# Kernel optimization log

Hardware: AMD Instinct MI355X
Metric: run time of the kernel (lower is better)

The kernel has to match this reference:

```python
import jax, jax.numpy as jnp
import numpy as np

T = 512          # tokens
H = 2048         # hidden_size
E = 256          # n_routed_experts (8 groups x 32)
G = 8            # tucker groups
EPG = 32         # experts per group
K = 6            # top_k
I = 1408         # moe_intermediate_size
R1 = 128         # tucker input rank
R2 = 128         # tucker output rank


def setup_inputs() -> dict:
    key = jax.random.key(0)
    ks = jax.random.split(key, 12)
    s = 0.02
    return {
        "hidden_states": jax.random.normal(ks[0], (T, H), jnp.float32),
        "w_router": jax.random.normal(ks[1], (H, E), jnp.float32) * s,
        # gate_proj Tucker factors: H -> I
        "U_in_gate": jax.random.normal(ks[2], (G, H, R1), jnp.float32) * s,
        "core_gate": jax.random.normal(ks[3], (E, R1, R2), jnp.float32) * s,
        "U_out_gate": jax.random.normal(ks[4], (G, I, R2), jnp.float32) * s,
        # up_proj Tucker factors: H -> I
        "U_in_up": jax.random.normal(ks[5], (G, H, R1), jnp.float32) * s,
        "core_up": jax.random.normal(ks[6], (E, R1, R2), jnp.float32) * s,
        "U_out_up": jax.random.normal(ks[7], (G, I, R2), jnp.float32) * s,
        # down_proj Tucker factors: I -> H
        "U_in_down": jax.random.normal(ks[8], (G, I, R1), jnp.float32) * s,
        "core_down": jax.random.normal(ks[9], (E, R1, R2), jnp.float32) * s,
        "U_out_down": jax.random.normal(ks[10], (G, H, R2), jnp.float32) * s,
    }


def _tucker_apply(x, g, e, U_in, core, U_out):
    """Per-expert Tucker linear: y_t = ((x_t @ U_in[g_t]) @ core[e_t]) @ U_out[g_t].T
    x: [Td, din]; g: [Td] group ids; e: [Td] full expert ids.
    U_in: [G, din, r1]; core: [E, r1, r2]; U_out: [G, dout, r2]."""
    h1 = jnp.einsum('td,gdr->tgr', x, U_in)                       # [Td, G, r1]
    h1 = jnp.take_along_axis(h1, g[:, None, None], axis=1)[:, 0]  # [Td, r1]
    h2 = jnp.einsum('tr,trs->ts', h1, core[e])                    # [Td, r2]
    y = jnp.einsum('ts,gds->tgd', h2, U_out)                      # [Td, G, dout]
    return jnp.take_along_axis(y, g[:, None, None], axis=1)[:, 0]


def reference(hidden_states, w_router, U_in_gate, core_gate, U_out_gate,
              U_in_up, core_up, U_out_up, U_in_down, core_down, U_out_down):
    n_tok, hid = hidden_states.shape
    router_logits = hidden_states @ w_router                          # [T, E]
    probs = jax.nn.softmax(router_logits.astype(jnp.float32), axis=-1)
    routing_weights, selected = jax.lax.top_k(probs, K)               # [T, K]
    routing_weights = routing_weights / routing_weights.sum(-1, keepdims=True)
    routing_weights = routing_weights.astype(hidden_states.dtype)

    xd = jnp.repeat(hidden_states, K, axis=0)                         # [T*K, H]
    e = selected.reshape(-1)                                          # [T*K]
    g = e // EPG                                                      # group ids

    gate_out = _tucker_apply(xd, g, e, U_in_gate, core_gate, U_out_gate)
    up_out = _tucker_apply(xd, g, e, U_in_up, core_up, U_out_up)
    inter = jax.nn.silu(gate_out) * up_out                            # [T*K, I]
    down_out = _tucker_apply(inter, g, e, U_in_down, core_down, U_out_down)

    combined = (down_out.reshape(n_tok, K, hid) * routing_weights[..., None]).sum(axis=1)
    return combined
```

## Files before the change

### kernel.cpp

```cpp
#include <hip/hip_runtime.h>
#include <cmath>
#include <cstdint>

#define TNUM 512
#define HID 2048
#define NEXP 256
#define NGRP 8
#define KTOP 6
#define IDIM 1408
#define RNK 128
#define NPAIR (TNUM*KTOP)
#define NRCAP 3328
#define MAXTILES (NRCAP/32)

typedef _Float16 f16;
typedef f16  f16x8 __attribute__((ext_vector_type(8)));
typedef f16  f16x4 __attribute__((ext_vector_type(4)));
typedef float f32x4 __attribute__((ext_vector_type(4)));
#define MFMA16(a,b,c) __builtin_amdgcn_mfma_f32_16x16x32_f16((a),(b),(c),0,0,0)

static __device__ __forceinline__ float4 ld4(const float* p){ return *reinterpret_cast<const float4*>(p); }
static __device__ __forceinline__ void st4(float* p, float4 v){ *reinterpret_cast<float4*>(p) = v; }
static __device__ __forceinline__ f16x8 ldh8(const f16* p){ return *reinterpret_cast<const f16x8*>(p); }

constexpr size_t A256(size_t x){ return (x + 255) & ~(size_t)255; }
constexpr size_t OFF_SEL    = 0;
constexpr size_t OFF_WT     = A256(OFF_SEL    + (size_t)NPAIR*4);
constexpr size_t OFF_CNT    = A256(OFF_WT     + (size_t)NPAIR*4);
constexpr size_t OFF_ESTART = A256(OFF_CNT    + (size_t)NEXP*4);
constexpr size_t OFF_ECUR   = A256(OFF_ESTART + (size_t)NEXP*4);
constexpr size_t OFF_TG     = A256(OFF_ECUR   + (size_t)NEXP*4);
constexpr size_t OFF_HDR    = A256(OFF_TG     + (size_t)MAXTILES*4);
constexpr size_t OFF_ROWT   = A256(OFF_HDR    + 16);
constexpr size_t OFF_POS    = A256(OFF_ROWT   + (size_t)NRCAP*4);
constexpr size_t OFF_BIG    = A256(OFF_POS    + (size_t)NPAIR*4);

constexpr size_t SZ_XH    = (size_t)TNUM*HID*2;
constexpr size_t SZ_UTI   = (size_t)NGRP*RNK*HID*2;
constexpr size_t SZ_CT    = (size_t)NEXP*RNK*RNK*2;
constexpr size_t SZ_H1ALL = (size_t)2*TNUM*NGRP*RNK*2;
constexpr size_t SZ_UO    = (size_t)NGRP*IDIM*RNK*2;
constexpr size_t SZ_UOD   = (size_t)NGRP*HID*RNK*2;
constexpr size_t SZ_H2    = (size_t)NRCAP*RNK*2;
constexpr size_t SZ_INTER = (size_t)NRCAP*IDIM*2;
constexpr size_t SZ_DOWNO = (size_t)NRCAP*HID*4;

constexpr size_t OFF_XH    = OFF_BIG;
constexpr size_t OFF_UTIG  = OFF_XH   + SZ_XH;
constexpr size_t OFF_UTIU  = OFF_UTIG + SZ_UTI;
constexpr size_t OFF_CGT   = OFF_UTIU + SZ_UTI;
constexpr size_t OFF_CUT   = OFF_CGT  + SZ_CT;
constexpr size_t OFF_H1    = OFF_CUT  + SZ_CT;
constexpr size_t REG_END   = OFF_H1   + SZ_H1ALL;
constexpr size_t OFF_INTER = OFF_XH;
constexpr size_t OFF_DOWNO = OFF_XH;
constexpr size_t OFF_LPART = OFF_H1;
constexpr size_t OFF_UOG   = REG_END;
constexpr size_t OFF_UOU   = OFF_UOG  + SZ_UO;
constexpr size_t OFF_UTID  = OFF_UOU  + SZ_UO;
constexpr size_t OFF_UOD   = OFF_UTID + SZ_UO;
constexpr size_t OFF_CDT   = OFF_UOD  + SZ_UOD;
constexpr size_t OFF_H2G   = OFF_CDT  + SZ_CT;
constexpr size_t OFF_H2U   = OFF_H2G  + SZ_H2;
constexpr size_t OFF_D1    = OFF_H2U  + SZ_H2;
constexpr size_t OFF_D2    = OFF_D1   + SZ_H2;
constexpr size_t WS_NEED   = OFF_D2   + SZ_H2;
static_assert(OFF_DOWNO + SZ_DOWNO <= OFF_UOG, "downo overlay must end before persistent tail");
static_assert(OFF_INTER + SZ_INTER <= OFF_CGT, "inter overlay must end before cores");

__global__ __launch_bounds__(256) void k_cvt_all(
    const float* __restrict__ x,   const float* __restrict__ Uog,
    const float* __restrict__ Uou, const float* __restrict__ Uod,
    f16* __restrict__ xh, f16* __restrict__ uog, f16* __restrict__ uou, f16* __restrict__ uod){
  const int b = blockIdx.x, tid = threadIdx.x;
  const float* in; f16* hi; size_t i; float scale;
  if(b < 1024){        in = x;   hi = xh;  i = (size_t)b*256 + tid;        scale = 1.f; }
  else if(b < 2432){   in = Uog; hi = uog; i = (size_t)(b-1024)*256 + tid; scale = 16.f; }
  else if(b < 3840){   in = Uou; hi = uou; i = (size_t)(b-2432)*256 + tid; scale = 16.f; }
  else {               in = Uod; hi = uod; i = (size_t)(b-3840)*256 + tid; scale = 16.f; }
  float4 v = ld4(in + i*4);
  f16x4 H;
  H[0]=(f16)(v.x*scale); H[1]=(f16)(v.y*scale); H[2]=(f16)(v.z*scale); H[3]=(f16)(v.w*scale);
  *reinterpret_cast<f16x4*>(hi + i*4) = H;
}

__global__ __launch_bounds__(256) void k_cvt_t3(
    const float* __restrict__ Uig, const float* __restrict__ Uiu, const float* __restrict__ Uid,
    f16* __restrict__ ig, f16* __restrict__ iu, f16* __restrict__ idn){
  __shared__ float tile[32][33];
  const int z = blockIdx.z, tensor = z>>3, g = z&7;
  const float* in; f16* hi; int R;
  if(tensor == 0){ in = Uig; hi = ig; R = HID; }
  else if(tensor == 1){ in = Uiu; hi = iu; R = HID; }
  else { in = Uid; hi = idn; R = IDIM; }
  const int r0 = blockIdx.y*32, c0 = blockIdx.x*32;
  if(r0 >= R) return;
  const int tid = threadIdx.x;
  { const int r = tid>>3, c4 = (tid&7)*4;
    float4 v = ld4(in + ((size_t)g*R + r0 + r)*RNK + c0 + c4);
    tile[r][c4]=v.x; tile[r][c4+1]=v.y; tile[r][c4+2]=v.z; tile[r][c4+3]=v.w; }
  __syncthreads();
  { const int c = tid>>3, r4 = (tid&7)*4;
    f16x4 H;
    #pragma unroll
    for(int k = 0; k < 4; k++) H[k] = (f16)(tile[r4+k][c]*16.f);
    *reinterpret_cast<f16x4*>(hi + ((size_t)g*RNK + c0 + c)*R + r0 + r4) = H; }
}

__global__ __launch_bounds__(256) void k_cvt_core(
    const float* __restrict__ cg, const float* __restrict__ cu, const float* __restrict__ cd,
    f16* __restrict__ cgt, f16* __restrict__ cut, f16* __restrict__ cdt){
  __shared__ float tile[32][33];
  const int z = blockIdx.z, tensor = z>>8, e = z&255;
  const float* in; f16* o;
  if(tensor == 0){ in = cg; o = cgt; }
  else if(tensor == 1){ in = cu; o = cut; }
  else { in = cd; o = cdt; }
  in += (size_t)e*RNK*RNK; o += (size_t)e*RNK*RNK;
  const int r0 = blockIdx.y*32, c0 = blockIdx.x*32;
  const int tid = threadIdx.x;
  { const int r = tid>>3, c4 = (tid&7)*4;
    float4 v = ld4(in + (size_t)(r0+r)*RNK + c0 + c4);
    tile[r][c4]=v.x; tile[r][c4+1]=v.y; tile[r][c4+2]=v.z; tile[r][c4+3]=v.w; }
  __syncthreads();
  { const int c = tid>>3, r4 = (tid&7)*4;
    f16x4 H;
    #pragma unroll
    for(int k = 0; k < 4; k++) H[k] = (f16)(tile[r4+k][c]*16.f);
    *reinterpret_cast<f16x4*>(o + (size_t)(c0+c)*RNK + r0 + r4) = H; }
}

__global__ __launch_bounds__(256) void k_router4(const float* __restrict__ x,
                                                 const float* __restrict__ w,
                                                 float* __restrict__ lpart){
  __shared__ float As[32][68];
  __shared__ float Bs[64][64];
  const int tid = threadIdx.x;
  const int t0 = blockIdx.x*32, e0 = blockIdx.y*64, kz = blockIdx.z;
  const int kb = kz*512;
  const int tx = tid & 15, ty = tid >> 4;
  float acc[2][4] = {{0.f}};
  for(int kc = 0; kc < 512; kc += 64){
    { const int r = tid>>3, k4 = (tid&7)<<2;
      st4(&As[r][k4],      ld4(&x[(size_t)(t0+r)*HID + kb + kc + k4]));
      st4(&As[r][k4+32],   ld4(&x[(size_t)(t0+r)*HID + kb + kc + k4 + 32])); }
    #pragma unroll
    for(int i = 0; i < 4; i++){ int idx = tid + i*256; int kr = idx>>4, e4 = (idx&15)<<2;
      st4(&Bs[kr][e4], ld4(&w[(size_t)(kb+kc+kr)*NEXP + e0 + e4])); }
    __syncthreads();
    for(int kk = 0; kk < 64; kk++){
      float4 b = ld4(&Bs[kk][tx<<2]);
      float a0 = As[(ty<<1)][kk], a1 = As[(ty<<1)+1][kk];
      acc[0][0] += a0*b.x; acc[0][1] += a0*b.y; acc[0][2] += a0*b.z; acc[0][3] += a0*b.w;
      acc[1][0] += a1*b.x; acc[1][1] += a1*b.y; acc[1][2] += a1*b.z; acc[1][3] += a1*b.w;
    }
    __syncthreads();
  }
  #pragma unroll
  for(int r = 0; r < 2; r++)
    st4(&lpart[((size_t)kz*TNUM + t0 + (ty<<1) + r)*NEXP + e0 + (tx<<2)],
        make_float4(acc[r][0],acc[r][1],acc[r][2],acc[r][3]));
}

__global__ __launch_bounds__(256) void k_topk(const float* __restrict__ lpart,
                                              int* __restrict__ sel,
                                              float* __restrict__ wt,
                                              int* __restrict__ cnt){
  __shared__ float wv[4];
  __shared__ int   wi[4];
  __shared__ float swin[KTOP];
  __shared__ int   iwin[KTOP];
  const int t = blockIdx.x, tid = threadIdx.x;
  const int lane = tid & 63, wid = tid >> 6;
  const size_t base = (size_t)t*NEXP + tid;
  float v = lpart[base] + lpart[base + (size_t)TNUM*NEXP]
          + lpart[base + (size_t)2*TNUM*NEXP] + lpart[base + (size_t)3*TNUM*NEXP];
  for(int k = 0; k < KTOP; k++){
    float cv = v; int ci = tid;
    #pragma unroll
    for(int off = 1; off < 64; off <<= 1){
      float ov = __shfl_xor(cv, off);
      int   oi = __shfl_xor(ci, off);
      if(ov > cv || (ov == cv && oi < ci)){ cv = ov; ci = oi; }
    }
    if(lane == 0){ wv[wid] = cv; wi[wid] = ci; }
    __syncthreads();
    if(tid == 0){
      float bv = wv[0]; int bi = wi[0];
      #pragma unroll
      for(int w2 = 1; w2 < 4; w2++)
        if(wv[w2] > bv || (wv[w2] == bv && wi[w2] < bi)){ bv = wv[w2]; bi = wi[w2]; }
      swin[k] = bv; iwin[k] = bi;
    }
    __syncthreads();
    if(tid == iwin[k]) v = -INFINITY;
  }
  if(tid == 0){
    float mx = swin[0], s = 0.f, ww[KTOP];
    #pragma unroll
    for(int k = 0; k < KTOP; k++){ ww[k] = expf(swin[k]-mx); s += ww[k]; }
    float inv = 1.f/s;
    #pragma unroll
    for(int k = 0; k < KTOP; k++){
      sel[t*KTOP+k] = iwin[k];
      wt[t*KTOP+k]  = ww[k]*inv;
      atomicAdd(&cnt[iwin[k]], 1);
    }
  }
}

__global__ __launch_bounds__(256) void k_meta(const int* __restrict__ cnt,
                                              int* __restrict__ estart,
                                              int* __restrict__ ecursor,
                                              int* __restrict__ tile_group,
                                              int* __restrict__ hdr){
  __shared__ int scnt[256];
  __shared__ int gsum[8];
  __shared__ int g0[9];
  const int tid = threadIdx.x;
  scnt[tid] = cnt[tid];
  if(tid < 8) gsum[tid] = 0;
  __syncthreads();
  atomicAdd(&gsum[tid>>5], scnt[tid]);
  __syncthreads();
  if(tid == 0){
    int run = 0;
    for(int g = 0; g < 8; g++){ g0[g] = run; run += (gsum[g]+31) & ~31; }
    g0[8] = run; hdr[0] = run>>5; hdr[1] = run;
  }
  __syncthreads();
  int g = tid >> 5, s = g0[g];
  for(int i = (g<<5); i < tid; i++) s += scnt[i];
  estart[tid] = s; ecursor[tid] = s;
  const int nt = g0[8] >> 5;
  for(int t2 = tid; t2 < MAXTILES; t2 += 256){
    int gg = -1;
    if(t2 < nt){
      for(int g2 = 0; g2 < 8; g2++) if(t2*32 >= g0[g2] && t2*32 < g0[g2+1]) gg = g2;
    }
    tile_group[t2] = gg;
  }
}

__global__ __launch_bounds__(256) void k_scatter(const int* __restrict__ sel,
                                                 int* __restrict__ ecursor,
                                                 int* __restrict__ row_t,
                                                 int* __restrict__ pos_of_pair){
  const int p = blockIdx.x*256 + threadIdx.x;
  if(p >= NPAIR) return;
  const int e = sel[p];
  const int pos = atomicAdd(&ecursor[e], 1);
  row_t[pos] = p / KTOP;
  pos_of_pair[p] = pos;
}

__global__ __launch_bounds__(256) void k_mm_stage1(
    const f16* __restrict__ xh,
    const f16* __restrict__ Bg_, const f16* __restrict__ Bu_,
    f16* __restrict__ H1){
  __shared__ float red[4][32][64];
  const int m = blockIdx.x, nt = blockIdx.y;
  const int pu = nt>>4, g = (nt>>1)&7, ch = nt&1;
  const f16* B = (pu ? Bu_ : Bg_) + (size_t)g*RNK*HID + (size_t)ch*64*HID;
  const int tid = threadIdx.x;
  const int wid = tid>>6, lane = tid&63, q = lane>>4, id = lane&15;
  const int kb = wid*512;
  const int r0 = m*32;
  f32x4 acc[2][4];
  #pragma unroll
  for(int f = 0; f < 2; f++)
    #pragma unroll
    for(int c = 0; c < 4; c++) acc[f][c] = (f32x4){0.f,0.f,0.f,0.f};
  #pragma unroll 4
  for(int kk = 0; kk < 512; kk += 32){
    f16x8 a0 = ldh8(xh + (size_t)(r0+id)*HID    + kb + kk + q*8);
    f16x8 a1 = ldh8(xh + (size_t)(r0+16+id)*HID + kb + kk + q*8);
    #pragma unroll
    for(int c = 0; c < 4; c++){
      f16x8 b = ldh8(B + (size_t)(c*16+id)*HID + kb + kk + q*8);
      acc[0][c] = MFMA16(a0, b, acc[0][c]);
      acc[1][c] = MFMA16(a1, b, acc[1][c]);
    }
  }
  #pragma unroll
  for(int f = 0; f < 2; f++)
    #pragma unroll
    for(int c = 0; c < 4; c++)
      #pragma unroll
      for(int r = 0; r < 4; r++)
        red[wid][f*16 + q*4 + r][c*16 + id] = acc[f][c][r];
  __syncthreads();
  f16* out = H1 + (size_t)pu*TNUM*(NGRP*RNK);
  const int row = tid>>3, c8 = (tid&7)*8;
  f16x8 o8;
  #pragma unroll
  for(int j = 0; j < 8; j++)
    o8[j] = (f16)(red[0][row][c8+j] + red[1][row][c8+j] + red[2][row][c8+j] + red[3][row][c8+j]);
  *reinterpret_cast<f16x8*>(&out[(size_t)(r0+row)*(NGRP*RNK) + g*RNK + ch*64 + c8]) = o8;
}

__global__ __launch_bounds__(256) void k_core2(
    const f16* __restrict__ Cg, const f16* __restrict__ Cu,
    const f16* __restrict__ H1,
    const int* __restrict__ estart, const int* __restrict__ cnt,
    const int* __restrict__ row_t,
    f16* __restrict__ h2g, f16* __restrict__ h2u){
  const int e = blockIdx.x, up = blockIdx.y;
  const int n = cnt[e];
  if(n == 0) return;
  const int j0 = estart[e], g = e >> 5;
  const f16* C = (up ? Cu : Cg) + (size_t)e*RNK*RNK;
  const f16* A = H1 + (size_t)up*TNUM*(NGRP*RNK);
  f16* o = up ? h2u : h2g;
  const int tid = threadIdx.x;
  const int wid = tid>>6, lane = tid&63, q = lane>>4, id = lane&15;
  for(int rt = 0; rt*16 < n; rt++){
    const int jrow = j0 + rt*16 + id;
    const int jj = jrow < j0+n ? jrow : j0;
    const f16* arow = A + (size_t)row_t[jj]*(NGRP*RNK) + g*RNK;
    f32x4 acc0 = (f32x4){0.f,0.f,0.f,0.f};
    f32x4 acc1 = (f32x4){0.f,0.f,0.f,0.f};
    #pragma unroll
    for(int kk = 0; kk < RNK; kk += 32){
      f16x8 a = ldh8(arow + kk + q*8);
      f16x8 b0 = ldh8(C + (size_t)(wid*32 + id)*RNK      + kk + q*8);
      f16x8 b1 = ldh8(C + (size_t)(wid*32 + 16 + id)*RNK + kk + q*8);
      acc0 = MFMA16(a, b0, acc0);
      acc1 = MFMA16(a, b1, acc1);
    }
    #pragma unroll
    for(int r = 0; r < 4; r++){
      const int j = j0 + rt*16 + q*4 + r;
      if(j < j0+n){
        o[(size_t)j*RNK + wid*32 + id]      = (f16)acc0[r];
        o[(size_t)j*RNK + wid*32 + 16 + id] = (f16)acc1[r];
      }
    }
  }
}

__global__ __launch_bounds__(128) void k_mm_gateup(
    const f16* __restrict__ Ag, const f16* __restrict__ Au,
    const f16* __restrict__ Bg, const f16* __restrict__ Bu,
    const int* __restrict__ tg,
    f16* __restrict__ inter){
  const int g = tg[blockIdx.x];
  if(g < 0) return;
  const int j0 = blockIdx.x*32;
  const int tid = threadIdx.x;
  const int wid = tid>>6, lane = tid&63, q = lane>>4, id = lane&15;
  const int c0 = blockIdx.y*128 + wid*64;
  const size_t bbase = (size_t)g*IDIM*RNK;
  f32x4 accg[2][4], accu[2][4];
  #pragma unroll
  for(int f = 0; f < 2; f++)
    #pragma unroll
    for(int c = 0; c < 4; c++){ accg[f][c] = (f32x4){0.f,0.f,0.f,0.f}; accu[f][c] = (f32x4){0.f,0.f,0.f,0.f}; }
  #pragma unroll 2
  for(int kk = 0; kk < RNK; kk += 32){
    const size_t a0off = (size_t)(j0+id)*RNK    + kk + q*8;
    const size_t a1off = (size_t)(j0+16+id)*RNK + kk + q*8;
    f16x8 ag0 = ldh8(Ag + a0off), ag1 = ldh8(Ag + a1off);
    f16x8 au0 = ldh8(Au + a0off), au1 = ldh8(Au + a1off);
    #pragma unroll
    for(int c = 0; c < 4; c++){
      const size_t boff = bbase + (size_t)(c0 + c*16 + id)*RNK + kk + q*8;
      f16x8 bg = ldh8(Bg + boff);
      f16x8 bu = ldh8(Bu + boff);
      accg[0][c] = MFMA16(ag0, bg, accg[0][c]);
      accg[1][c] = MFMA16(ag1, bg, accg[1][c]);
      accu[0][c] = MFMA16(au0, bu, accu[0][c]);
      accu[1][c] = MFMA16(au1, bu, accu[1][c]);
    }
  }
  #pragma unroll
  for(int f = 0; f < 2; f++)
    #pragma unroll
    for(int c = 0; c < 4; c++)
      #pragma unroll
      for(int r = 0; r < 4; r++){
        float vg = accg[f][c][r] * (1.f/4096.f);
        float vu = accu[f][c][r] * (1.f/4096.f);
        float sv = vg/(1.f+expf(-vg))*vu*256.f;
        inter[(size_t)(j0 + f*16 + q*4 + r)*IDIM + c0 + c*16 + id] = (f16)sv;
      }
}

__global__ __launch_bounds__(256) void k_mm_down_in(
    const f16* __restrict__ A_, const f16* __restrict__ B_,
    const int* __restrict__ tg,
    f16* __restrict__ d1){
  __shared__ float red[4][32][64];
  const int g = tg[blockIdx.x];
  if(g < 0) return;
  const int j0 = blockIdx.x*32;
  const int ch = blockIdx.y;
  const f16* B = B_ + (size_t)g*RNK*IDIM + (size_t)ch*64*IDIM;
  const int tid = threadIdx.x;
  const int wid = tid>>6, lane = tid&63, q = lane>>4, id = lane&15;
  const int kb = wid*352;
  f32x4 acc[2][4];
  #pragma unroll
  for(int f = 0; f < 2; f++)
    #pragma unroll
    for(int c = 0; c < 4; c++) acc[f][c] = (f32x4){0.f,0.f,0.f,0.f};
  #pragma unroll 2
  for(int kk = 0; kk < 352; kk += 32){
    f16x8 a0 = ldh8(A_ + (size_t)(j0+id)*IDIM    + kb + kk + q*8);
    f16x8 a1 = ldh8(A_ + (size_t)(j0+16+id)*IDIM + kb + kk + q*8);
    #pragma unroll
    for(int c = 0; c < 4; c++){
      f16x8 b = ldh8(B + (size_t)(c*16+id)*IDIM + kb + kk + q*8);
      acc[0][c] = MFMA16(a0, b, acc[0][c]);
      acc[1][c] = MFMA16(a1, b, acc[1][c]);
    }
  }
  #pragma unroll
  for(int f = 0; f < 2; f++)
    #pragma unroll
    for(int c = 0; c < 4; c++)
      #pragma unroll
      for(int r = 0; r < 4; r++)
        red[wid][f*16 + q*4 + r][c*16 + id] = acc[f][c][r];
  __syncthreads();
  const int row = tid>>3, c8 = (tid&7)*8;
  f16x8 o8;
  #pragma unroll
  for(int j = 0; j < 8; j++)
    o8[j] = (f16)(red[0][row][c8+j] + red[1][row][c8+j] + red[2][row][c8+j] + red[3][row][c8+j]);
  *reinterpret_cast<f16x8*>(&d1[(size_t)(j0+row)*RNK + ch*64 + c8]) = o8;
}

__global__ __launch_bounds__(256) void k_core_down(
    const f16* __restrict__ Cd,
    const f16* __restrict__ d1,
    const int* __restrict__ estart, const int* __restrict__ cnt,
    f16* __restrict__ d2){
  const int e = blockIdx.x;
  const int n = cnt[e];
  if(n == 0) return;
  const int j0 = estart[e];
  const f16* C = Cd + (size_t)e*RNK*RNK;
  const int tid = threadIdx.x;
  const int wid = tid>>6, lane = tid&63, q = lane>>4, id = lane&15;
  for(int rt = 0; rt*16 < n; rt++){
    const int jrow = j0 + rt*16 + id;
    const int jj = jrow < j0+n ? jrow : j0;
    const f16* arow = d1 + (size_t)jj*RNK;
    f32x4 acc0 = (f32x4){0.f,0.f,0.f,0.f};
    f32x4 acc1 = (f32x4){0.f,0.f,0.f,0.f};
    #pragma unroll
    for(int kk = 0; kk < RNK; kk += 32){
      f16x8 a = ldh8(arow + kk + q*8);
      f16x8 b0 = ldh8(C + (size_t)(wid*32 + id)*RNK      + kk + q*8);
      f16x8 b1 = ldh8(C + (size_t)(wid*32 + 16 + id)*RNK + kk + q*8);
      acc0 = MFMA16(a, b0, acc0);
      acc1 = MFMA16(a, b1, acc1);
    }
    #pragma unroll
    for(int r = 0; r < 4; r++){
      const int j = j0 + rt*16 + q*4 + r;
      if(j < j0+n){
        d2[(size_t)j*RNK + wid*32 + id]      = (f16)acc0[r];
        d2[(size_t)j*RNK + wid*32 + 16 + id] = (f16)acc1[r];
      }
    }
  }
}

__global__ __launch_bounds__(128) void k_mm_down_out(
    const f16* __restrict__ A_, const f16* __restrict__ B_,
    const int* __restrict__ tg,
    float* __restrict__ downo){
  const int g = tg[blockIdx.x];
  if(g < 0) return;
  const int j0 = blockIdx.x*32;
  const f16* B = B_ + (size_t)g*HID*RNK;
  const int tid = threadIdx.x;
  const int wid = tid>>6, lane = tid&63, q = lane>>4, id = lane&15;
  const int c0 = blockIdx.y*128 + wid*64;
  f32x4 acc[2][4];
  #pragma unroll
  for(int f = 0; f < 2; f++)
    #pragma unroll
    for(int c = 0; c < 4; c++) acc[f][c] = (f32x4){0.f,0.f,0.f,0.f};
  #pragma unroll 2
  for(int kk = 0; kk < RNK; kk += 32){
    f16x8 a0 = ldh8(A_ + (size_t)(j0+id)*RNK    + kk + q*8);
    f16x8 a1 = ldh8(A_ + (size_t)(j0+16+id)*RNK + kk + q*8);
    #pragma unroll
    for(int c = 0; c < 4; c++){
      f16x8 b = ldh8(B + (size_t)(c0 + c*16 + id)*RNK + kk + q*8);
      acc[0][c] = MFMA16(a0, b, acc[0][c]);
      acc[1][c] = MFMA16(a1, b, acc[1][c]);
    }
  }
  #pragma unroll
  for(int f = 0; f < 2; f++)
    #pragma unroll
    for(int c = 0; c < 4; c++)
      #pragma unroll
      for(int r = 0; r < 4; r++)
        downo[(size_t)(j0 + f*16 + q*4 + r)*HID + c0 + c*16 + id] = acc[f][c][r]*(1.f/1048576.f);
}

__global__ __launch_bounds__(256) void k_combine(const float* __restrict__ downo,
                                                 const int* __restrict__ pos_of_pair,
                                                 const float* __restrict__ wt,
                                                 float* __restrict__ out){
  const int idx = blockIdx.x*256 + threadIdx.x;
  const int t  = idx >> 9;
  const int h4 = (idx & 511) << 2;
  float4 acc = make_float4(0.f,0.f,0.f,0.f);
  #pragma unroll
  for(int k = 0; k < KTOP; k++){
    const int p = t*KTOP + k;
    const float w = wt[p];
    const int pos = pos_of_pair[p];
    float4 v = ld4(&downo[(size_t)pos*HID + h4]);
    acc.x += w*v.x; acc.y += w*v.y; acc.z += w*v.z; acc.w += w*v.w;
  }
  st4(&out[(size_t)t*HID + h4], acc);
}

extern "C" void kernel_launch(void* const* d_in, const int* in_sizes, int n_in,
                              void* d_out, int out_size, void* d_ws, size_t ws_size,
                              hipStream_t stream){
  const float* x   = (const float*)d_in[0];
  const float* wr  = (const float*)d_in[1];
  const float* Uig = (const float*)d_in[2];
  const float* cg  = (const float*)d_in[3];
  const float* Uog = (const float*)d_in[4];
  const float* Uiu = (const float*)d_in[5];
  const float* cu  = (const float*)d_in[6];
  const float* Uou = (const float*)d_in[7];
  const float* Uid = (const float*)d_in[8];
  const float* cd  = (const float*)d_in[9];
  const float* Uod = (const float*)d_in[10];
  float* out = (float*)d_out;
  char* ws = (char*)d_ws;
  if(ws_size < WS_NEED) return;

  int*   sel    = (int*)  (ws + OFF_SEL);
  float* wt     = (float*)(ws + OFF_WT);
  int*   cnt    = (int*)  (ws + OFF_CNT);
  int*   estart = (int*)  (ws + OFF_ESTART);
  int*   ecur   = (int*)  (ws + OFF_ECUR);
  int*   tg     = (int*)  (ws + OFF_TG);
  int*   hdr    = (int*)  (ws + OFF_HDR);
  int*   row_t  = (int*)  (ws + OFF_ROWT);
  int*   pos    = (int*)  (ws + OFF_POS);
  float* lpart  = (float*)(ws + OFF_LPART);
  f16* xh    = (f16*)(ws + OFF_XH);
  f16* utig  = (f16*)(ws + OFF_UTIG);
  f16* utiu  = (f16*)(ws + OFF_UTIU);
  f16* cgt   = (f16*)(ws + OFF_CGT);
  f16* cut   = (f16*)(ws + OFF_CUT);
  f16* cdt   = (f16*)(ws + OFF_CDT);
  f16* H1    = (f16*)(ws + OFF_H1);
  f16* uog   = (f16*)(ws + OFF_UOG);
  f16* uou   = (f16*)(ws + OFF_UOU);
  f16* utid  = (f16*)(ws + OFF_UTID);
  f16* uod   = (f16*)(ws + OFF_UOD);
  f16* h2g   = (f16*)(ws + OFF_H2G);
  f16* h2u   = (f16*)(ws + OFF_H2U);
  f16* inter = (f16*)(ws + OFF_INTER);
  f16* d1    = (f16*)(ws + OFF_D1);
  f16* d2    = (f16*)(ws + OFF_D2);
  float* downo = (float*)(ws + OFF_DOWNO);

  hipMemsetAsync(cnt, 0, NEXP*sizeof(int), stream);

  k_router4  <<<dim3(16,4,4),      256, 0, stream>>>(x, wr, lpart);
  k_topk     <<<TNUM,              256, 0, stream>>>(lpart, sel, wt, cnt);
  k_meta     <<<1,                 256, 0, stream>>>(cnt, estart, ecur, tg, hdr);
  k_scatter  <<<12,                256, 0, stream>>>(sel, ecur, row_t, pos);

  k_cvt_all  <<<5888,              256, 0, stream>>>(x, Uog, Uou, Uod, xh, uog, uou, uod);
  k_cvt_t3   <<<dim3(4,64,24),     256, 0, stream>>>(Uig, Uiu, Uid, utig, utiu, utid);
  k_cvt_core <<<dim3(4,4,768),     256, 0, stream>>>(cg, cu, cd, cgt, cut, cdt);

  k_mm_stage1<<<dim3(16,32),       256, 0, stream>>>(xh, utig, utiu, H1);
  k_core2    <<<dim3(NEXP,2),      256, 0, stream>>>(cgt, cut, H1, estart, cnt, row_t, h2g, h2u);
  k_mm_gateup<<<dim3(MAXTILES,11), 128, 0, stream>>>(h2g, h2u, uog, uou, tg, inter);
  k_mm_down_in<<<dim3(MAXTILES,2), 256, 0, stream>>>(inter, utid, tg, d1);
  k_core_down<<<NEXP,              256, 0, stream>>>(cdt, d1, estart, cnt, d2);
  k_mm_down_out<<<dim3(MAXTILES,16),128,0, stream>>>(d2, uod, tg, downo);
  k_combine  <<<1024,              256, 0, stream>>>(downo, pos, wt, out);
}
```

Before: 155.7 us.

## Use split-fp16 MFMA router, fuse meta/scatter, fold combine into down_out atomics

Replaces the fp32 scalar router GEMM with an MFMA version that splits x and w_router into fp16 hi/lo pairs, using three products to keep near-fp32 accuracy for top-k selection. It adds a transposed hi/lo router weight conversion. It merges the meta and scatter kernels into one block that scatters row weights instead of pair positions. It removes the fp32 downo buffer and the combine kernel by having down_out atomically add weighted results into a zeroed output. This trades extra conversion work and atomic contention for less memory traffic and fewer launches, and makes the summation order nondeterministic.

```diff
diff --git a/kernel.cpp b/kernel.cpp
--- a/kernel.cpp
+++ b/kernel.cpp
@@ -28,12 +28,11 @@
 constexpr size_t OFF_WT     = A256(OFF_SEL    + (size_t)NPAIR*4);
 constexpr size_t OFF_CNT    = A256(OFF_WT     + (size_t)NPAIR*4);
 constexpr size_t OFF_ESTART = A256(OFF_CNT    + (size_t)NEXP*4);
-constexpr size_t OFF_ECUR   = A256(OFF_ESTART + (size_t)NEXP*4);
-constexpr size_t OFF_TG     = A256(OFF_ECUR   + (size_t)NEXP*4);
+constexpr size_t OFF_TG     = A256(OFF_ESTART + (size_t)NEXP*4);
 constexpr size_t OFF_HDR    = A256(OFF_TG     + (size_t)MAXTILES*4);
 constexpr size_t OFF_ROWT   = A256(OFF_HDR    + 16);
-constexpr size_t OFF_POS    = A256(OFF_ROWT   + (size_t)NRCAP*4);
-constexpr size_t OFF_BIG    = A256(OFF_POS    + (size_t)NPAIR*4);
+constexpr size_t OFF_ROWW   = A256(OFF_ROWT   + (size_t)NRCAP*4);
+constexpr size_t OFF_BIG    = A256(OFF_ROWW   + (size_t)NRCAP*4);
 
 constexpr size_t SZ_XH    = (size_t)TNUM*HID*2;
 constexpr size_t SZ_UTI   = (size_t)NGRP*RNK*HID*2;
@@ -41,47 +40,82 @@
 constexpr size_t SZ_H1ALL = (size_t)2*TNUM*NGRP*RNK*2;
 constexpr size_t SZ_UO    = (size_t)NGRP*IDIM*RNK*2;
 constexpr size_t SZ_UOD   = (size_t)NGRP*HID*RNK*2;
+constexpr size_t SZ_WR    = (size_t)NEXP*HID*2;
 constexpr size_t SZ_H2    = (size_t)NRCAP*RNK*2;
 constexpr size_t SZ_INTER = (size_t)NRCAP*IDIM*2;
-constexpr size_t SZ_DOWNO = (size_t)NRCAP*HID*4;
 
 constexpr size_t OFF_XH    = OFF_BIG;
-constexpr size_t OFF_UTIG  = OFF_XH   + SZ_XH;
+constexpr size_t OFF_XL    = OFF_XH   + SZ_XH;
+constexpr size_t OFF_UTIG  = OFF_XL   + SZ_XH;
 constexpr size_t OFF_UTIU  = OFF_UTIG + SZ_UTI;
 constexpr size_t OFF_CGT   = OFF_UTIU + SZ_UTI;
 constexpr size_t OFF_CUT   = OFF_CGT  + SZ_CT;
 constexpr size_t OFF_H1    = OFF_CUT  + SZ_CT;
 constexpr size_t REG_END   = OFF_H1   + SZ_H1ALL;
 constexpr size_t OFF_INTER = OFF_XH;
-constexpr size_t OFF_DOWNO = OFF_XH;
 constexpr size_t OFF_LPART = OFF_H1;
 constexpr size_t OFF_UOG   = REG_END;
 constexpr size_t OFF_UOU   = OFF_UOG  + SZ_UO;
 constexpr size_t OFF_UTID  = OFF_UOU  + SZ_UO;
 constexpr size_t OFF_UOD   = OFF_UTID + SZ_UO;
 constexpr size_t OFF_CDT   = OFF_UOD  + SZ_UOD;
-constexpr size_t OFF_H2G   = OFF_CDT  + SZ_CT;
+constexpr size_t OFF_WRH   = OFF_CDT  + SZ_CT;
+constexpr size_t OFF_WRL   = OFF_WRH  + SZ_WR;
+constexpr size_t OFF_H2G   = OFF_WRL  + SZ_WR;
 constexpr size_t OFF_H2U   = OFF_H2G  + SZ_H2;
 constexpr size_t OFF_D1    = OFF_H2U  + SZ_H2;
 constexpr size_t OFF_D2    = OFF_D1   + SZ_H2;
 constexpr size_t WS_NEED   = OFF_D2   + SZ_H2;
-static_assert(OFF_DOWNO + SZ_DOWNO <= OFF_UOG, "downo overlay must end before persistent tail");
 static_assert(OFF_INTER + SZ_INTER <= OFF_CGT, "inter overlay must end before cores");
+static_assert(SZ_H1ALL >= (size_t)4*TNUM*NEXP*4/2 || true, "");
 
 __global__ __launch_bounds__(256) void k_cvt_all(
     const float* __restrict__ x,   const float* __restrict__ Uog,
     const float* __restrict__ Uou, const float* __restrict__ Uod,
-    f16* __restrict__ xh, f16* __restrict__ uog, f16* __restrict__ uou, f16* __restrict__ uod){
+    f16* __restrict__ xh, f16* __restrict__ xl,
+    f16* __restrict__ uog, f16* __restrict__ uou, f16* __restrict__ uod){
   const int b = blockIdx.x, tid = threadIdx.x;
-  const float* in; f16* hi; size_t i; float scale;
-  if(b < 1024){        in = x;   hi = xh;  i = (size_t)b*256 + tid;        scale = 1.f; }
-  else if(b < 2432){   in = Uog; hi = uog; i = (size_t)(b-1024)*256 + tid; scale = 16.f; }
-  else if(b < 3840){   in = Uou; hi = uou; i = (size_t)(b-2432)*256 + tid; scale = 16.f; }
-  else {               in = Uod; hi = uod; i = (size_t)(b-3840)*256 + tid; scale = 16.f; }
+  if(b < 1024){
+    const size_t i = (size_t)b*256 + tid;
+    float4 v = ld4(x + i*4);
+    f16x4 H, L;
+    H[0]=(f16)v.x; L[0]=(f16)(v.x-(float)H[0]);
+    H[1]=(f16)v.y; L[1]=(f16)(v.y-(float)H[1]);
+    H[2]=(f16)v.z; L[2]=(f16)(v.z-(float)H[2]);
+    H[3]=(f16)v.w; L[3]=(f16)(v.w-(float)H[3]);
+    *reinterpret_cast<f16x4*>(xh + i*4) = H;
+    *reinterpret_cast<f16x4*>(xl + i*4) = L;
+    return;
+  }
+  const float* in; f16* hi; size_t i;
+  if(b < 2432){        in = Uog; hi = uog; i = (size_t)(b-1024)*256 + tid; }
+  else if(b < 3840){   in = Uou; hi = uou; i = (size_t)(b-2432)*256 + tid; }
+  else {               in = Uod; hi = uod; i = (size_t)(b-3840)*256 + tid; }
   float4 v = ld4(in + i*4);
   f16x4 H;
-  H[0]=(f16)(v.x*scale); H[1]=(f16)(v.y*scale); H[2]=(f16)(v.z*scale); H[3]=(f16)(v.w*scale);
+  H[0]=(f16)(v.x*16.f); H[1]=(f16)(v.y*16.f); H[2]=(f16)(v.z*16.f); H[3]=(f16)(v.w*16.f);
   *reinterpret_cast<f16x4*>(hi + i*4) = H;
+}
+
+__global__ __launch_bounds__(256) void k_cvt_wr(const float* __restrict__ w,
+                                                f16* __restrict__ wh, f16* __restrict__ wl){
+  __shared__ float tile[32][33];
+  const int r0 = blockIdx.y*32, c0 = blockIdx.x*32;
+  const int tid = threadIdx.x;
+  { const int r = tid>>3, c4 = (tid&7)*4;
+    float4 v = ld4(w + (size_t)(r0+r)*NEXP + c0 + c4);
+    tile[r][c4]=v.x; tile[r][c4+1]=v.y; tile[r][c4+2]=v.z; tile[r][c4+3]=v.w; }
+  __syncthreads();
+  { const int c = tid>>3, r4 = (tid&7)*4;
+    f16x4 H, L;
+    #pragma unroll
+    for(int k = 0; k < 4; k++){
+      float v = tile[r4+k][c]*16.f;
+      H[k] = (f16)v; L[k] = (f16)(v - (float)H[k]);
+    }
+    const size_t o = (size_t)(c0+c)*HID + r0 + r4;
+    *reinterpret_cast<f16x4*>(wh + o) = H;
+    *reinterpret_cast<f16x4*>(wl + o) = L; }
 }
 
 __global__ __launch_bounds__(256) void k_cvt_t3(
@@ -130,36 +164,56 @@
     *reinterpret_cast<f16x4*>(o + (size_t)(c0+c)*RNK + r0 + r4) = H; }
 }
 
-__global__ __launch_bounds__(256) void k_router4(const float* __restrict__ x,
-                                                 const float* __restrict__ w,
-                                                 float* __restrict__ lpart){
-  __shared__ float As[32][68];
-  __shared__ float Bs[64][64];
-  const int tid = threadIdx.x;
-  const int t0 = blockIdx.x*32, e0 = blockIdx.y*64, kz = blockIdx.z;
-  const int kb = kz*512;
-  const int tx = tid & 15, ty = tid >> 4;
-  float acc[2][4] = {{0.f}};
-  for(int kc = 0; kc < 512; kc += 64){
-    { const int r = tid>>3, k4 = (tid&7)<<2;
-      st4(&As[r][k4],      ld4(&x[(size_t)(t0+r)*HID + kb + kc + k4]));
-      st4(&As[r][k4+32],   ld4(&x[(size_t)(t0+r)*HID + kb + kc + k4 + 32])); }
-    #pragma unroll
-    for(int i = 0; i < 4; i++){ int idx = tid + i*256; int kr = idx>>4, e4 = (idx&15)<<2;
-      st4(&Bs[kr][e4], ld4(&w[(size_t)(kb+kc+kr)*NEXP + e0 + e4])); }
-    __syncthreads();
-    for(int kk = 0; kk < 64; kk++){
-      float4 b = ld4(&Bs[kk][tx<<2]);
-      float a0 = As[(ty<<1)][kk], a1 = As[(ty<<1)+1][kk];
-      acc[0][0] += a0*b.x; acc[0][1] += a0*b.y; acc[0][2] += a0*b.z; acc[0][3] += a0*b.w;
-      acc[1][0] += a1*b.x; acc[1][1] += a1*b.y; acc[1][2] += a1*b.z; acc[1][3] += a1*b.w;
-    }
-    __syncthreads();
-  }
-  #pragma unroll
-  for(int r = 0; r < 2; r++)
-    st4(&lpart[((size_t)kz*TNUM + t0 + (ty<<1) + r)*NEXP + e0 + (tx<<2)],
-        make_float4(acc[r][0],acc[r][1],acc[r][2],acc[r][3]));
+__global__ __launch_bounds__(256) void k_router_mfma(
+    const f16* __restrict__ xh, const f16* __restrict__ xl,
+    const f16* __restrict__ wh, const f16* __restrict__ wl,
+    float* __restrict__ lpart){
+  __shared__ float red[4][32][64];
+  const int m = blockIdx.x, ecol = blockIdx.y, kz = blockIdx.z;
+  const int tid = threadIdx.x;
+  const int wid = tid>>6, lane = tid&63, q = lane>>4, id = lane&15;
+  const int r0 = m*32, e0 = ecol*64;
+  const int kb = kz*512 + wid*128;
+  f32x4 acc[2][4];
+  #pragma unroll
+  for(int f = 0; f < 2; f++)
+    #pragma unroll
+    for(int c = 0; c < 4; c++) acc[f][c] = (f32x4){0.f,0.f,0.f,0.f};
+  #pragma unroll
+  for(int kk = 0; kk < 128; kk += 32){
+    const size_t a0 = (size_t)(r0+id)*HID    + kb + kk + q*8;
+    const size_t a1 = (size_t)(r0+16+id)*HID + kb + kk + q*8;
+    f16x8 ah0 = ldh8(xh + a0), al0 = ldh8(xl + a0);
+    f16x8 ah1 = ldh8(xh + a1), al1 = ldh8(xl + a1);
+    #pragma unroll
+    for(int c = 0; c < 4; c++){
+      const size_t bo = (size_t)(e0 + c*16 + id)*HID + kb + kk + q*8;
+      f16x8 bh = ldh8(wh + bo);
+      f16x8 bl = ldh8(wl + bo);
+      acc[0][c] = MFMA16(ah0, bh, acc[0][c]);
+      acc[0][c] = MFMA16(ah0, bl, acc[0][c]);
+      acc[0][c] = MFMA16(al0, bh, acc[0][c]);
+      acc[1][c] = MFMA16(ah1, bh, acc[1][c]);
+      acc[1][c] = MFMA16(ah1, bl, acc[1][c]);
+      acc[1][c] = MFMA16(al1, bh, acc[1][c]);
+    }
+  }
+  #pragma unroll
+  for(int f = 0; f < 2; f++)
+    #pragma unroll
+    for(int c = 0; c < 4; c++)
+      #pragma unroll
+      for(int r = 0; r < 4; r++)
+        red[wid][f*16 + q*4 + r][c*16 + id] = acc[f][c][r];
+  __syncthreads();
+  const int row = tid>>3, c8 = (tid&7)*8;
+  float o[8];
+  #pragma unroll
+  for(int j = 0; j < 8; j++)
+    o[j] = (red[0][row][c8+j] + red[1][row][c8+j] + red[2][row][c8+j] + red[3][row][c8+j])*0.0625f;
+  float* dst = &lpart[((size_t)kz*TNUM + r0 + row)*NEXP + e0 + c8];
+  st4(dst,     make_float4(o[0],o[1],o[2],o[3]));
+  st4(dst + 4, make_float4(o[4],o[5],o[6],o[7]));
 }
 
 __global__ __launch_bounds__(256) void k_topk(const float* __restrict__ lpart,
@@ -209,14 +263,14 @@
   }
 }
 
-__global__ __launch_bounds__(256) void k_meta(const int* __restrict__ cnt,
-                                              int* __restrict__ estart,
-                                              int* __restrict__ ecursor,
-                                              int* __restrict__ tile_group,
-                                              int* __restrict__ hdr){
+__global__ __launch_bounds__(256) void k_meta_scatter(
+    const int* __restrict__ cnt, const int* __restrict__ sel, const float* __restrict__ wt,
+    int* __restrict__ estart, int* __restrict__ tile_group, int* __restrict__ hdr,
+    int* __restrict__ row_t, float* __restrict__ row_w){
   __shared__ int scnt[256];
   __shared__ int gsum[8];
   __shared__ int g0[9];
+  __shared__ int curs[256];
   const int tid = threadIdx.x;
   scnt[tid] = cnt[tid];
   if(tid < 8) gsum[tid] = 0;
@@ -231,7 +285,7 @@
   __syncthreads();
   int g = tid >> 5, s = g0[g];
   for(int i = (g<<5); i < tid; i++) s += scnt[i];
-  estart[tid] = s; ecursor[tid] = s;
+  estart[tid] = s; curs[tid] = s;
   const int nt = g0[8] >> 5;
   for(int t2 = tid; t2 < MAXTILES; t2 += 256){
     int gg = -1;
@@ -240,18 +294,14 @@
     }
     tile_group[t2] = gg;
   }
-}
-
-__global__ __launch_bounds__(256) void k_scatter(const int* __restrict__ sel,
-                                                 int* __restrict__ ecursor,
-                                                 int* __restrict__ row_t,
-                                                 int* __restrict__ pos_of_pair){
-  const int p = blockIdx.x*256 + threadIdx.x;
-  if(p >= NPAIR) return;
-  const int e = sel[p];
-  const int pos = atomicAdd(&ecursor[e], 1);
-  row_t[pos] = p / KTOP;
-  pos_of_pair[p] = pos;
+  for(int i = tid; i < NRCAP; i += 256) row_w[i] = 0.f;
+  __syncthreads();
+  for(int p = tid; p < NPAIR; p += 256){
+    const int e = sel[p];
+    const int pos = atomicAdd(&curs[e], 1);
+    row_t[pos] = p / KTOP;
+    row_w[pos] = wt[p];
+  }
 }
 
 __global__ __launch_bounds__(256) void k_mm_stage1(
@@ -471,7 +521,8 @@
 __global__ __launch_bounds__(128) void k_mm_down_out(
     const f16* __restrict__ A_, const f16* __restrict__ B_,
     const int* __restrict__ tg,
-    float* __restrict__ downo){
+    const int* __restrict__ row_t, const float* __restrict__ row_w,
+    float* __restrict__ out){
   const int g = tg[blockIdx.x];
   if(g < 0) return;
   const int j0 = blockIdx.x*32;
@@ -498,29 +549,16 @@
   #pragma unroll
   for(int f = 0; f < 2; f++)
     #pragma unroll
-    for(int c = 0; c < 4; c++)
-      #pragma unroll
-      for(int r = 0; r < 4; r++)
-        downo[(size_t)(j0 + f*16 + q*4 + r)*HID + c0 + c*16 + id] = acc[f][c][r]*(1.f/1048576.f);
-}
-
-__global__ __launch_bounds__(256) void k_combine(const float* __restrict__ downo,
-                                                 const int* __restrict__ pos_of_pair,
-                                                 const float* __restrict__ wt,
-                                                 float* __restrict__ out){
-  const int idx = blockIdx.x*256 + threadIdx.x;
-  const int t  = idx >> 9;
-  const int h4 = (idx & 511) << 2;
-  float4 acc = make_float4(0.f,0.f,0.f,0.f);
-  #pragma unroll
-  for(int k = 0; k < KTOP; k++){
-    const int p = t*KTOP + k;
-    const float w = wt[p];
-    const int pos = pos_of_pair[p];
-    float4 v = ld4(&downo[(size_t)pos*HID + h4]);
-    acc.x += w*v.x; acc.y += w*v.y; acc.z += w*v.z; acc.w += w*v.w;
-  }
-  st4(&out[(size_t)t*HID + h4], acc);
+    for(int r = 0; r < 4; r++){
+      const int j = j0 + f*16 + q*4 + r;
+      const float w = row_w[j];
+      if(w != 0.f){
+        const size_t obase = (size_t)row_t[j]*HID;
+        #pragma unroll
+        for(int c = 0; c < 4; c++)
+          atomicAdd(&out[obase + c0 + c*16 + id], acc[f][c][r]*w*(1.f/1048576.f));
+      }
+    }
 }
 
 extern "C" void kernel_launch(void* const* d_in, const int* in_sizes, int n_in,
@@ -545,13 +583,13 @@
   float* wt     = (float*)(ws + OFF_WT);
   int*   cnt    = (int*)  (ws + OFF_CNT);
   int*   estart = (int*)  (ws + OFF_ESTART);
-  int*   ecur   = (int*)  (ws + OFF_ECUR);
   int*   tg     = (int*)  (ws + OFF_TG);
   int*   hdr    = (int*)  (ws + OFF_HDR);
   int*   row_t  = (int*)  (ws + OFF_ROWT);
-  int*   pos    = (int*)  (ws + OFF_POS);
+  float* row_w  = (float*)(ws + OFF_ROWW);
   float* lpart  = (float*)(ws + OFF_LPART);
   f16* xh    = (f16*)(ws + OFF_XH);
+  f16* xl    = (f16*)(ws + OFF_XL);
   f16* utig  = (f16*)(ws + OFF_UTIG);
   f16* utiu  = (f16*)(ws + OFF_UTIU);
   f16* cgt   = (f16*)(ws + OFF_CGT);
@@ -562,21 +600,24 @@
   f16* uou   = (f16*)(ws + OFF_UOU);
   f16* utid  = (f16*)(ws + OFF_UTID);
   f16* uod   = (f16*)(ws + OFF_UOD);
+  f16* wrh   = (f16*)(ws + OFF_WRH);
+  f16* wrl   = (f16*)(ws + OFF_WRL);
   f16* h2g   = (f16*)(ws + OFF_H2G);
   f16* h2u   = (f16*)(ws + OFF_H2U);
   f16* inter = (f16*)(ws + OFF_INTER);
   f16* d1    = (f16*)(ws + OFF_D1);
   f16* d2    = (f16*)(ws + OFF_D2);
-  float* downo = (float*)(ws + OFF_DOWNO);
 
   hipMemsetAsync(cnt, 0, NEXP*sizeof(int), stream);
-
-  k_router4  <<<dim3(16,4,4),      256, 0, stream>>>(x, wr, lpart);
+  hipMemsetAsync(out, 0, (size_t)TNUM*HID*sizeof(float), stream);
+
+  k_cvt_all  <<<5888,              256, 0, stream>>>(x, Uog, Uou, Uod, xh, xl, uog, uou, uod);
+  k_cvt_wr   <<<dim3(8,64),        256, 0, stream>>>(wr, wrh, wrl);
+
+  k_router_mfma<<<dim3(16,4,4),    256, 0, stream>>>(xh, xl, wrh, wrl, lpart);
   k_topk     <<<TNUM,              256, 0, stream>>>(lpart, sel, wt, cnt);
-  k_meta     <<<1,                 256, 0, stream>>>(cnt, estart, ecur, tg, hdr);
-  k_scatter  <<<12,                256, 0, stream>>>(sel, ecur, row_t, pos);
-
-  k_cvt_all  <<<5888,              256, 0, stream>>>(x, Uog, Uou, Uod, xh, uog, uou, uod);
+  k_meta_scatter<<<1,              256, 0, stream>>>(cnt, sel, wt, estart, tg, hdr, row_t, row_w);
+
   k_cvt_t3   <<<dim3(4,64,24),     256, 0, stream>>>(Uig, Uiu, Uid, utig, utiu, utid);
   k_cvt_core <<<dim3(4,4,768),     256, 0, stream>>>(cg, cu, cd, cgt, cut, cdt);
 
@@ -585,6 +626,5 @@
   k_mm_gateup<<<dim3(MAXTILES,11), 128, 0, stream>>>(h2g, h2u, uog, uou, tg, inter);
   k_mm_down_in<<<dim3(MAXTILES,2), 256, 0, stream>>>(inter, utid, tg, d1);
   k_core_down<<<NEXP,              256, 0, stream>>>(cdt, d1, estart, cnt, d2);
-  k_mm_down_out<<<dim3(MAXTILES,16),128,0, stream>>>(d2, uod, tg, downo);
-  k_combine  <<<1024,              256, 0, stream>>>(downo, pos, wt, out);
-}
+  k_mm_down_out<<<dim3(MAXTILES,16),128,0, stream>>>(d2, uod, tg, row_t, row_w, out);
+}
```

Result: slower. 168.9 us (+8.5%).
